# Performance work log

Hardware: AMD Instinct MI355X
Metric: run time of the kernel (lower is better)

Reference implementation:

```python
import jax, jax.numpy as jnp
from jax import lax
import numpy as np

LRELU_SLOPE = 0.1
DILATIONS = (1, 2, 4)
B, C, T = 8, 256, 8192


def pd_indexing(x, d, dilation):
    """Pitch-dependent past/future gather along time.
    x: (B, C, T); d: (B, 1, T) float dilation factors.
    Returns xP, xF: (B, C, T), zero where index is out of range.
    """
    b, c, t_len = x.shape
    t = jnp.arange(t_len, dtype=x.dtype)  # (T,)
    dil = d[:, 0, :] * dilation           # (B, T)
    idxP = jnp.round(t[None, :] - dil).astype(jnp.int32)  # (B, T)
    idxF = jnp.round(t[None, :] + dil).astype(jnp.int32)  # (B, T)
    validP = (idxP >= 0).astype(x.dtype)[:, None, :]        # (B,1,T)
    validF = (idxF < t_len).astype(x.dtype)[:, None, :]
    idxPc = jnp.broadcast_to(jnp.clip(idxP, 0, t_len - 1)[:, None, :], (b, c, t_len))
    idxFc = jnp.broadcast_to(jnp.clip(idxF, 0, t_len - 1)[:, None, :], (b, c, t_len))
    xP = jnp.take_along_axis(x, idxPc, axis=2) * validP
    xF = jnp.take_along_axis(x, idxFc, axis=2) * validF
    return xP, xF


def conv1x1(x, w, bias):
    # x: (B,C,T), w: (O,C), bias: (O,)
    return jnp.einsum('oc,bct->bot', w, x) + bias[None, :, None]


def conv3(x, w, bias):
    # x: (B,C,T), w: (O,C,3), padding=1
    y = lax.conv_general_dilated(x, w, window_strides=(1,), padding=[(1, 1)],
                                 dimension_numbers=('NCH', 'OIH', 'NCH'))
    return y + bias[None, :, None]


def setup_inputs() -> dict:
    key = jax.random.key(0)
    ks = jax.random.split(key, 8)
    x = jax.random.normal(ks[0], (B, C, T), dtype=jnp.float32)
    d = jax.random.uniform(ks[1], (B, 1, T), dtype=jnp.float32, minval=0.0, maxval=16.0)
    n = len(DILATIONS)
    s1 = 1.0 / np.sqrt(C)
    s3 = 1.0 / np.sqrt(3 * C)
    WC = jax.random.normal(ks[2], (n, C, C), dtype=jnp.float32) * s1
    WP = jax.random.normal(ks[3], (n, C, C), dtype=jnp.float32) * s1
    WF = jax.random.normal(ks[4], (n, C, C), dtype=jnp.float32) * s1
    WA = jax.random.normal(ks[5], (n, C, C, 3), dtype=jnp.float32) * s3
    bC = jnp.zeros((n, C), dtype=jnp.float32)
    bP = jnp.zeros((n, C), dtype=jnp.float32)
    bF = jnp.zeros((n, C), dtype=jnp.float32)
    bA = jnp.zeros((n, C), dtype=jnp.float32)
    return {"x": x, "d": d, "WC": WC, "bC": bC, "WP": WP, "bP": bP,
            "WF": WF, "bF": bF, "WA": WA, "bA": bA}


def reference(x, d, WC, bC, WP, bP, WF, bF, WA, bA):
    for i, dilation in enumerate(DILATIONS):
        xt = jax.nn.leaky_relu(x, LRELU_SLOPE)
        xP, xF = pd_indexing(xt, d, dilation)
        xt = conv1x1(xt, WC[i], bC[i]) + conv1x1(xP, WP[i], bP[i]) + conv1x1(xF, WF[i], bF[i])
        xt = jax.nn.leaky_relu(xt, LRELU_SLOPE)
        xt = conv3(xt, WA[i], bA[i])
        x = xt + x
    return x
```

## Files before the change

kernel.cpp:

```cpp
#include <hip/hip_runtime.h>
#include <hip/hip_bf16.h>
#include <cstddef>
#include <cstdint>

constexpr int Bn = 8, Cn = 256, Tn = 8192;
constexpr int NL = 3;
constexpr int Kc = 768;
constexpr float SLOPE = 0.1f;

typedef unsigned short u16;
using bf8   = __attribute__((ext_vector_type(8))) short;
using f32x4 = __attribute__((ext_vector_type(4))) float;

__device__ __forceinline__ float lrelu(float v) { return v > 0.f ? v : SLOPE * v; }
__device__ __forceinline__ u16 f2bf(float f) {
    __hip_bfloat16 h = __float2bfloat16(f);
    return *reinterpret_cast<u16*>(&h);
}

__device__ __forceinline__ void g2l16(const u16* g, u16* l) {
    __builtin_amdgcn_global_load_lds(
        (const __attribute__((address_space(1))) char*)g,
        (__attribute__((address_space(3))) char*)l, 16, 0, 0);
}

__device__ __forceinline__ void pipe_barrier() {
    __builtin_amdgcn_s_barrier();
    __builtin_amdgcn_sched_barrier(0);
}

__global__ __launch_bounds__(256)
void k_wprep(const float* __restrict__ WC, const float* __restrict__ WP,
             const float* __restrict__ WF, const float* __restrict__ WA,
             const float* __restrict__ bC, const float* __restrict__ bP,
             const float* __restrict__ bF,
             u16* __restrict__ Wcat, u16* __restrict__ WAp, float* __restrict__ bSum,
             u16* __restrict__ zrow)
{
    if (blockIdx.x == 0) zrow[threadIdx.x] = 0;
    const int n1 = NL * Cn * Kc;
    for (int i = blockIdx.x * blockDim.x + threadIdx.x; i < n1;
         i += gridDim.x * blockDim.x) {
        int c = i % Cn;
        int s = (i / Cn) % 3;
        int o = (i / (3 * Cn)) % Cn;
        int l = i / (3 * Cn * Cn);
        size_t src = ((size_t)l * Cn + o) * Cn + c;
        float wc = (s == 0) ? WC[src] : (s == 1) ? WP[src] : WF[src];
        Wcat[i] = f2bf(wc);
        WAp[i] = f2bf(WA[src * 3 + s]);
    }
    for (int i = blockIdx.x * blockDim.x + threadIdx.x; i < NL * Cn;
         i += gridDim.x * blockDim.x)
        bSum[i] = bC[i] + bP[i] + bF[i];
}

__global__ __launch_bounds__(256)
void k_prep(const float* __restrict__ x, u16* __restrict__ xT)
{
    __shared__ float s[64][65];
    const int b = blockIdx.z, c0 = blockIdx.y * 64, t0 = blockIdx.x * 64;
    const int tid = threadIdx.x;
    const float* xb = x + ((size_t)b * Cn + c0) * Tn + t0;

    int tt = tid & 63, c4 = tid >> 6;
    for (int cc = c4; cc < 64; cc += 4)
        s[cc][tt] = xb[(size_t)cc * Tn + tt];
    __syncthreads();

    int ccS = tid & 63, t4 = tid >> 6;
    u16* xTb = xT + ((size_t)b * Tn + t0) * Cn + c0;
    for (int t2 = t4; t2 < 64; t2 += 4)
        xTb[(size_t)t2 * Cn + ccS] = f2bf(lrelu(s[ccS][t2]));
}

__global__ __launch_bounds__(256, 3)
void k_gemm1(const u16* __restrict__ xT, const float* __restrict__ d,
             const u16* __restrict__ Wl, const float* __restrict__ bS,
             float dil, u16* __restrict__ zT, const u16* __restrict__ zrow)
{
    __shared__ u16 smem[6 * 4096];
    __shared__ int sRow[3][128];

    const int tid = threadIdx.x;
    const int b = blockIdx.z;
    const int t0 = blockIdx.x * 128;
    const int o0 = blockIdx.y * 128;

    if (tid < 128) {
        int t = t0 + tid;
        float dv = d[(size_t)b * Tn + t] * dil;
        int ip = (int)rintf((float)t - dv);
        int iF = (int)rintf((float)t + dv);
        sRow[0][tid] = t;
        sRow[1][tid] = (ip >= 0) ? ip : -1;
        sRow[2][tid] = (iF < Tn) ? iF : -1;
    }
    __syncthreads();

    const int srow = tid >> 2;
    const int schunkL = (tid & 3) * 8;
    const int schunkG = ((tid & 3) ^ ((tid >> 3) & 3)) * 8;
    const u16* xTb = xT + (size_t)b * Tn * Cn;
    const char* xbc = (const char*)xTb;
    const int zoff = (int)((const char*)(zrow + schunkG) - xbc);

    int offX0[3], offX1[3];
    #pragma unroll
    for (int s = 0; s < 3; ++s) {
        int r0 = sRow[s][srow], r1 = sRow[s][srow + 64];
        offX0[s] = (r0 >= 0) ? (int)(((size_t)r0 * Cn + schunkG) * 2) : zoff;
        offX1[s] = (r1 >= 0) ? (int)(((size_t)r1 * Cn + schunkG) * 2) : zoff;
    }
    const u16* wbase = Wl + (size_t)(o0 + srow) * Kc + schunkG;

    const int lane = tid & 63, wv = tid >> 6;
    const int wm = (wv & 1) * 64;
    const int wn = (wv >> 1) * 64;
    const int lr = lane & 15, quad = lane >> 4;
    const int rchunk = (quad ^ ((lr >> 1) & 3)) * 8;

    const int ldsW = srow * 32 + schunkL;
    const int ldsW2 = (srow + 64) * 32 + schunkL;

    auto dma = [&](int kg, int bsel) {
        int seg = kg >> 3, kk = (kg & 7) * 32;
        u16* bx = smem + bsel * 4096;
        u16* bw = smem + 12288 + bsel * 4096;
        g2l16(wbase + seg * 256 + kk,                   bw + ldsW);
        g2l16(wbase + (size_t)64 * Kc + seg * 256 + kk, bw + ldsW2);
        g2l16((const u16*)(xbc + offX0[seg] + kk * 2), bx + ldsW);
        g2l16((const u16*)(xbc + offX1[seg] + kk * 2), bx + ldsW2);
    };

    f32x4 acc[4][4] = {};
    dma(0, 0); dma(1, 1);

    #pragma unroll
    for (int kg = 0; kg < 24; ++kg) {
        if (kg < 23)
            asm volatile("s_waitcnt vmcnt(4) lgkmcnt(0)" ::: "memory");
        else
            asm volatile("s_waitcnt vmcnt(0) lgkmcnt(0)" ::: "memory");
        pipe_barrier();

        const u16* bX = smem + (kg % 3) * 4096;
        const u16* bW = smem + 12288 + (kg % 3) * 4096;

        bf8 af[4], bg[4];
        #pragma unroll
        for (int mi = 0; mi < 4; ++mi)
            af[mi] = *(const bf8*)(bX + (wm + mi * 16 + lr) * 32 + rchunk);
        #pragma unroll
        for (int ni = 0; ni < 4; ++ni)
            bg[ni] = *(const bf8*)(bW + (wn + ni * 16 + lr) * 32 + rchunk);

        if (kg + 2 < 24) dma(kg + 2, (kg + 2) % 3);

        __builtin_amdgcn_s_setprio(1);
        #pragma unroll
        for (int mi = 0; mi < 4; ++mi)
            #pragma unroll
            for (int ni = 0; ni < 4; ++ni)
                acc[mi][ni] = __builtin_amdgcn_mfma_f32_16x16x32_bf16(
                    af[mi], bg[ni], acc[mi][ni], 0, 0, 0);
        __builtin_amdgcn_s_setprio(0);
    }

    float bias[4];
    #pragma unroll
    for (int ni = 0; ni < 4; ++ni) bias[ni] = bS[o0 + wn + ni * 16 + lr];
    u16* zTb = zT + (size_t)b * Tn * Cn;
    #pragma unroll
    for (int mi = 0; mi < 4; ++mi)
        #pragma unroll
        for (int r = 0; r < 4; ++r) {
            int t = t0 + wm + mi * 16 + quad * 4 + r;
            u16* row = zTb + (size_t)t * Cn + o0 + wn;
            #pragma unroll
            for (int ni = 0; ni < 4; ++ni)
                row[ni * 16 + lr] = f2bf(lrelu(acc[mi][ni][r] + bias[ni]));
        }
}

__global__ __launch_bounds__(256, 3)
void k_gemm2(const u16* __restrict__ zT, const u16* __restrict__ WAl,
             const float* __restrict__ bA, const float* __restrict__ xres,
             float* __restrict__ out, u16* __restrict__ xTn, int writeXT,
             const u16* __restrict__ zrow)
{
    __shared__ u16 smem[6 * 4096];

    const int tid = threadIdx.x;
    const int b = blockIdx.z;
    const int t0 = blockIdx.x * 128;
    const int o0 = blockIdx.y * 128;

    const int srow = tid >> 2;
    const int schunkL = (tid & 3) * 8;
    const int schunkG = ((tid & 3) ^ ((tid >> 3) & 3)) * 8;
    const int lane = tid & 63, wv = tid >> 6;
    const int wo = (wv & 1) * 64;
    const int wt = (wv >> 1) * 64;
    const int lr = lane & 15, quad = lane >> 4;
    const int rchunk = (quad ^ ((lr >> 1) & 3)) * 8;

    const u16* zTb = zT + (size_t)b * Tn * Cn;
    const char* zbc = (const char*)zTb;
    const int zoff = (int)((const char*)(zrow + schunkG) - zbc);

    int offZ0[3], offZ1[3];
    #pragma unroll
    for (int tap = 0; tap < 3; ++tap) {
        int r0 = t0 + srow + tap - 1;
        int r1 = r0 + 64;
        offZ0[tap] = (r0 >= 0 && r0 < Tn)
                         ? (int)(((size_t)r0 * Cn + schunkG) * 2) : zoff;
        offZ1[tap] = (r1 >= 0 && r1 < Tn)
                         ? (int)(((size_t)r1 * Cn + schunkG) * 2) : zoff;
    }
    const u16* wbase = WAl + (size_t)(o0 + srow) * Kc + schunkG;

    const int ldsW = srow * 32 + schunkL;
    const int ldsW2 = (srow + 64) * 32 + schunkL;

    auto dma = [&](int kg, int bsel) {
        int tap = kg >> 3, kk = (kg & 7) * 32;
        u16* bz = smem + bsel * 4096;
        u16* bw = smem + 12288 + bsel * 4096;
        g2l16(wbase + tap * 256 + kk,                   bw + ldsW);
        g2l16(wbase + (size_t)64 * Kc + tap * 256 + kk, bw + ldsW2);
        g2l16((const u16*)(zbc + offZ0[tap] + kk * 2), bz + ldsW);
        g2l16((const u16*)(zbc + offZ1[tap] + kk * 2), bz + ldsW2);
    };

    f32x4 acc[4][4] = {};
    dma(0, 0); dma(1, 1);

    #pragma unroll
    for (int kg = 0; kg < 24; ++kg) {
        if (kg < 23)
            asm volatile("s_waitcnt vmcnt(4) lgkmcnt(0)" ::: "memory");
        else
            asm volatile("s_waitcnt vmcnt(0) lgkmcnt(0)" ::: "memory");
        pipe_barrier();

        const u16* bZ = smem + (kg % 3) * 4096;
        const u16* bW = smem + 12288 + (kg % 3) * 4096;

        bf8 af[4], bg[4];
        #pragma unroll
        for (int mi = 0; mi < 4; ++mi)
            af[mi] = *(const bf8*)(bW + (wo + mi * 16 + lr) * 32 + rchunk);
        #pragma unroll
        for (int ni = 0; ni < 4; ++ni)
            bg[ni] = *(const bf8*)(bZ + (wt + ni * 16 + lr) * 32 + rchunk);

        if (kg + 2 < 24) dma(kg + 2, (kg + 2) % 3);

        __builtin_amdgcn_s_setprio(1);
        #pragma unroll
        for (int mi = 0; mi < 4; ++mi)
            #pragma unroll
            for (int ni = 0; ni < 4; ++ni)
                acc[mi][ni] = __builtin_amdgcn_mfma_f32_16x16x32_bf16(
                    af[mi], bg[ni], acc[mi][ni], 0, 0, 0);
        __builtin_amdgcn_s_setprio(0);
    }

    float biasv[4][4];
    #pragma unroll
    for (int mi = 0; mi < 4; ++mi) {
        float4 bb = *(const float4*)(bA + o0 + wo + mi * 16 + quad * 4);
        biasv[mi][0] = bb.x; biasv[mi][1] = bb.y; biasv[mi][2] = bb.z; biasv[mi][3] = bb.w;
    }

    if (writeXT) {
        u16* strip = smem + wv * 1152;
        u16* xTb2 = xTn + (size_t)b * Tn * Cn;
        #pragma unroll
        for (int ni = 0; ni < 4; ++ni) {
            __syncthreads();
            #pragma unroll
            for (int mi = 0; mi < 4; ++mi) {
                ushort4 pk;
                #pragma unroll
                for (int r = 0; r < 4; ++r) {
                    int o = o0 + wo + mi * 16 + quad * 4 + r;
                    size_t idx = ((size_t)b * Cn + o) * Tn + t0 + wt + ni * 16 + lr;
                    float v = acc[mi][ni][r] + biasv[mi][r] + xres[idx];
                    out[idx] = v;
                    ((u16*)&pk)[r] = f2bf(lrelu(v));
                }
                *(ushort4*)(strip + lr * 72 + mi * 16 + quad * 4) = pk;
            }
            __syncthreads();
            #pragma unroll
            for (int it = 0; it < 2; ++it) {
                int tt = (lane >> 3) + it * 8;
                uint4 vv = *(const uint4*)(strip + tt * 72 + (lane & 7) * 8);
                *(uint4*)(xTb2 + (size_t)(t0 + wt + ni * 16 + tt) * Cn
                          + o0 + wo + (lane & 7) * 8) = vv;
            }
        }
    } else {
        #pragma unroll
        for (int mi = 0; mi < 4; ++mi)
            #pragma unroll
            for (int r = 0; r < 4; ++r) {
                int o = o0 + wo + mi * 16 + quad * 4 + r;
                size_t base = ((size_t)b * Cn + o) * Tn + t0 + wt;
                #pragma unroll
                for (int ni = 0; ni < 4; ++ni) {
                    size_t idx = base + ni * 16 + lr;
                    out[idx] = acc[mi][ni][r] + biasv[mi][r] + xres[idx];
                }
            }
    }
}

extern "C" void kernel_launch(void* const* d_in, const int* in_sizes, int n_in,
                              void* d_out, int out_size, void* d_ws, size_t ws_size,
                              hipStream_t stream)
{
    const float* x  = (const float*)d_in[0];
    const float* d  = (const float*)d_in[1];
    const float* WC = (const float*)d_in[2];
    const float* bC = (const float*)d_in[3];
    const float* WP = (const float*)d_in[4];
    const float* bP = (const float*)d_in[5];
    const float* WF = (const float*)d_in[6];
    const float* bF = (const float*)d_in[7];
    const float* WA = (const float*)d_in[8];
    const float* bA = (const float*)d_in[9];
    float* out = (float*)d_out;

    char* ws = (char*)d_ws;
    u16*   xT   = (u16*)(ws);
    u16*   zT   = (u16*)(ws + (size_t)Bn * Tn * Cn * 2);
    u16*   Wcat = (u16*)(ws + (size_t)2 * Bn * Tn * Cn * 2);
    u16*   WAp  = Wcat + (size_t)NL * Cn * Kc;
    float* bSum = (float*)(WAp + (size_t)NL * Cn * Kc);
    u16*   zrow = (u16*)(bSum + NL * Cn);

    k_wprep<<<dim3(1024), dim3(256), 0, stream>>>(WC, WP, WF, WA, bC, bP, bF,
                                                  Wcat, WAp, bSum, zrow);

    dim3 gP(Tn / 64, Cn / 64, Bn);
    dim3 gG(Tn / 128, Cn / 128, Bn);
    dim3 blk(256);

    k_prep<<<gP, blk, 0, stream>>>(x, xT);

    const float dils[NL] = {1.f, 2.f, 4.f};
    const float* xcur = x;
    for (int i = 0; i < NL; ++i) {
        k_gemm1<<<gG, blk, 0, stream>>>(xT, d,
                                        Wcat + (size_t)i * Cn * Kc,
                                        bSum + (size_t)i * Cn,
                                        dils[i], zT, zrow);
        k_gemm2<<<gG, blk, 0, stream>>>(zT,
                                        WAp + (size_t)i * Cn * Kc,
                                        bA + (size_t)i * Cn,
                                        xcur, out, xT, (i < NL - 1) ? 1 : 0,
                                        zrow);
        xcur = out;
    }
}
```

Measured before the change: 396.8 us.

## Fuse gather-GEMM and conv3 GEMM into one kernel with LDS-resident z tile

Merges the two per-layer GEMM kernels into one 512-thread block that covers all 256 output channels for a 128-step time tile. The first GEMM also computes the two halo rows, and its activated result stays in swizzled LDS as the input to the 3-tap conv GEMM. This removes the zT round trip through global memory and one launch per layer. In exchange each block recomputes the halo rows, holds more LDS and registers, runs a smaller grid with lower occupancy, and ping-pongs the xT buffers. The xT epilogue now writes 8-byte scattered stores instead of staging through LDS for coalesced 16-byte stores.

```diff
diff --git a/kernel.cpp b/kernel.cpp
--- a/kernel.cpp
+++ b/kernel.cpp
@@ -74,88 +74,211 @@
         xTb[(size_t)t2 * Cn + ccS] = f2bf(lrelu(s[ccS][t2]));
 }
 
-__global__ __launch_bounds__(256, 3)
-void k_gemm1(const u16* __restrict__ xT, const float* __restrict__ d,
+constexpr int SLOT = 12800;
+constexpr int ZOFF = 3 * SLOT;
+constexpr int ZSZ  = 130 * 256;
+
+__global__ __launch_bounds__(512, 2)
+void k_fused(const u16* __restrict__ xTsrc, const float* __restrict__ d,
              const u16* __restrict__ Wl, const float* __restrict__ bS,
-             float dil, u16* __restrict__ zT, const u16* __restrict__ zrow)
+             const u16* __restrict__ WAl, const float* __restrict__ bA,
+             float dil, const float* __restrict__ xres, float* __restrict__ out,
+             u16* __restrict__ xTn, int writeXT, const u16* __restrict__ zrow)
 {
-    __shared__ u16 smem[6 * 4096];
-    __shared__ int sRow[3][128];
+    __shared__ u16 smem[ZOFF + ZSZ];
+    __shared__ int sRow[3][130];
 
     const int tid = threadIdx.x;
     const int b = blockIdx.z;
     const int t0 = blockIdx.x * 128;
-    const int o0 = blockIdx.y * 128;
-
-    if (tid < 128) {
-        int t = t0 + tid;
-        float dv = d[(size_t)b * Tn + t] * dil;
-        int ip = (int)rintf((float)t - dv);
-        int iF = (int)rintf((float)t + dv);
-        sRow[0][tid] = t;
-        sRow[1][tid] = (ip >= 0) ? ip : -1;
-        sRow[2][tid] = (iF < Tn) ? iF : -1;
+
+    if (tid < 130) {
+        int tz = t0 - 1 + tid;
+        if (tz < 0 || tz >= Tn) {
+            sRow[0][tid] = -1; sRow[1][tid] = -1; sRow[2][tid] = -1;
+        } else {
+            float dv = d[(size_t)b * Tn + tz] * dil;
+            int ip = (int)rintf((float)tz - dv);
+            int iF = (int)rintf((float)tz + dv);
+            sRow[0][tid] = tz;
+            sRow[1][tid] = (ip >= 0) ? ip : -1;
+            sRow[2][tid] = (iF < Tn) ? iF : -1;
+        }
     }
     __syncthreads();
 
+    const int lane = tid & 63, wv = tid >> 6;
     const int srow = tid >> 2;
-    const int schunkL = (tid & 3) * 8;
-    const int schunkG = ((tid & 3) ^ ((tid >> 3) & 3)) * 8;
-    const u16* xTb = xT + (size_t)b * Tn * Cn;
+    const int sg  = ((tid & 3) ^ ((tid >> 3) & 3)) * 8;
+    const int sg2 = ((lane & 3) ^ ((lane >> 3) & 3)) * 8;
+
+    const u16* xTb = xTsrc + (size_t)b * Tn * Cn;
     const char* xbc = (const char*)xTb;
-    const int zoff = (int)((const char*)(zrow + schunkG) - xbc);
-
-    int offX0[3], offX1[3];
+    const int zoffA = (int)((const char*)(zrow + sg) - xbc);
+    const int zoffB = (int)((const char*)(zrow + sg2) - xbc);
+
+    int offX[3];
     #pragma unroll
     for (int s = 0; s < 3; ++s) {
-        int r0 = sRow[s][srow], r1 = sRow[s][srow + 64];
-        offX0[s] = (r0 >= 0) ? (int)(((size_t)r0 * Cn + schunkG) * 2) : zoff;
-        offX1[s] = (r1 >= 0) ? (int)(((size_t)r1 * Cn + schunkG) * 2) : zoff;
-    }
-    const u16* wbase = Wl + (size_t)(o0 + srow) * Kc + schunkG;
-
-    const int lane = tid & 63, wv = tid >> 6;
-    const int wm = (wv & 1) * 64;
-    const int wn = (wv >> 1) * 64;
+        int r = sRow[s][srow];
+        offX[s] = (r >= 0) ? (int)((r * Cn + sg) * 2) : zoffA;
+    }
+    int offX2[3] = { zoffB, zoffB, zoffB };
+    if (wv == 7) {
+        int j = lane >> 2;
+        if (j < 2) {
+            #pragma unroll
+            for (int s = 0; s < 3; ++s) {
+                int r = sRow[s][128 + j];
+                offX2[s] = (r >= 0) ? (int)((r * Cn + sg2) * 2) : zoffB;
+            }
+        }
+    }
+    const u16* wbase1 = Wl  + (size_t)srow * Kc + sg;
+    const u16* wbase2 = WAl + (size_t)srow * Kc + sg;
+
+    const int mo  = (wv & 3) * 64;
+    const int wzr = (wv >> 2) * 64;
+    const bool heavy = (wzr == 64);
     const int lr = lane & 15, quad = lane >> 4;
     const int rchunk = (quad ^ ((lr >> 1) & 3)) * 8;
 
-    const int ldsW = srow * 32 + schunkL;
-    const int ldsW2 = (srow + 64) * 32 + schunkL;
-
-    auto dma = [&](int kg, int bsel) {
+    auto dma1 = [&](int kg, int slot) {
         int seg = kg >> 3, kk = (kg & 7) * 32;
-        u16* bx = smem + bsel * 4096;
-        u16* bw = smem + 12288 + bsel * 4096;
-        g2l16(wbase + seg * 256 + kk,                   bw + ldsW);
-        g2l16(wbase + (size_t)64 * Kc + seg * 256 + kk, bw + ldsW2);
-        g2l16((const u16*)(xbc + offX0[seg] + kk * 2), bx + ldsW);
-        g2l16((const u16*)(xbc + offX1[seg] + kk * 2), bx + ldsW2);
+        u16* bw = smem + slot * SLOT;
+        u16* bx = bw + 8192;
+        if (wv == 7)
+            g2l16((const u16*)(xbc + offX2[seg] + kk * 2), bx + 4096 + lane * 8);
+        g2l16(wbase1 + seg * 256 + kk,                    bw + tid * 8);
+        g2l16(wbase1 + (size_t)128 * Kc + seg * 256 + kk, bw + 4096 + tid * 8);
+        g2l16((const u16*)(xbc + offX[seg] + kk * 2),     bx + tid * 8);
     };
-
-    f32x4 acc[4][4] = {};
-    dma(0, 0); dma(1, 1);
+    auto dma2 = [&](int kg, int slot) {
+        u16* bw = smem + slot * SLOT;
+        g2l16(wbase2 + kg * 32,                    bw + tid * 8);
+        g2l16(wbase2 + (size_t)128 * Kc + kg * 32, bw + 4096 + tid * 8);
+    };
+
+    const f32x4 zv4 = {0.f, 0.f, 0.f, 0.f};
+    f32x4 acc[4][5];
+    #pragma unroll
+    for (int mi = 0; mi < 4; ++mi)
+        #pragma unroll
+        for (int ni = 0; ni < 5; ++ni) acc[mi][ni] = zv4;
+
+    dma1(0, 0); dma1(1, 1);
 
     #pragma unroll
     for (int kg = 0; kg < 24; ++kg) {
-        if (kg < 23)
-            asm volatile("s_waitcnt vmcnt(4) lgkmcnt(0)" ::: "memory");
-        else
-            asm volatile("s_waitcnt vmcnt(0) lgkmcnt(0)" ::: "memory");
+        if (kg < 23) {
+            if (wv == 7) asm volatile("s_waitcnt vmcnt(4) lgkmcnt(0)" ::: "memory");
+            else         asm volatile("s_waitcnt vmcnt(3) lgkmcnt(0)" ::: "memory");
+        } else {
+            asm volatile("s_waitcnt vmcnt(2) lgkmcnt(0)" ::: "memory");
+        }
         pipe_barrier();
 
-        const u16* bX = smem + (kg % 3) * 4096;
-        const u16* bW = smem + 12288 + (kg % 3) * 4096;
-
+        const u16* bW = smem + (kg % 3) * SLOT;
+        const u16* bX = bW + 8192;
+        bf8 af[4], bg[4], bg4 = {};
+        #pragma unroll
+        for (int mi = 0; mi < 4; ++mi)
+            af[mi] = *(const bf8*)(bW + (mo + mi * 16 + lr) * 32 + rchunk);
+        #pragma unroll
+        for (int ni = 0; ni < 4; ++ni)
+            bg[ni] = *(const bf8*)(bX + (wzr + ni * 16 + lr) * 32 + rchunk);
+        if (heavy)
+            bg4 = *(const bf8*)(bX + (128 + lr) * 32 + rchunk);
+
+        if (kg + 2 < 24) dma1(kg + 2, (kg + 2) % 3);
+        else             dma2(kg - 22, (kg - 22) % 3);
+
+        __builtin_amdgcn_s_setprio(1);
+        #pragma unroll
+        for (int mi = 0; mi < 4; ++mi)
+            #pragma unroll
+            for (int ni = 0; ni < 4; ++ni)
+                acc[mi][ni] = __builtin_amdgcn_mfma_f32_16x16x32_bf16(
+                    af[mi], bg[ni], acc[mi][ni], 0, 0, 0);
+        if (heavy) {
+            #pragma unroll
+            for (int mi = 0; mi < 4; ++mi)
+                acc[mi][4] = __builtin_amdgcn_mfma_f32_16x16x32_bf16(
+                    af[mi], bg4, acc[mi][4], 0, 0, 0);
+        }
+        __builtin_amdgcn_s_setprio(0);
+    }
+
+    u16* zsm = smem + ZOFF;
+    {
+        float4 bSv[4];
+        #pragma unroll
+        for (int mi = 0; mi < 4; ++mi)
+            bSv[mi] = *(const float4*)(bS + mo + mi * 16 + quad * 4);
+
+        #pragma unroll
+        for (int ni = 0; ni < 4; ++ni) {
+            int zr = wzr + ni * 16 + lr;
+            int tz = t0 - 1 + zr;
+            bool vz = (tz >= 0) && (tz < Tn);
+            #pragma unroll
+            for (int mi = 0; mi < 4; ++mi) {
+                int ob = mo + mi * 16 + quad * 4;
+                ushort4 pk;
+                #pragma unroll
+                for (int r = 0; r < 4; ++r) {
+                    float v = acc[mi][ni][r] + ((const float*)&bSv[mi])[r];
+                    ((u16*)&pk)[r] = vz ? f2bf(lrelu(v)) : (u16)0;
+                }
+                int zi = zr * 256 + ((((ob >> 3) ^ (zr & 7)) << 3) | (ob & 7));
+                *(ushort4*)(zsm + zi) = pk;
+            }
+        }
+        if (heavy && lr < 2) {
+            int zr = 128 + lr;
+            int tz = t0 - 1 + zr;
+            bool vz = (tz >= 0) && (tz < Tn);
+            #pragma unroll
+            for (int mi = 0; mi < 4; ++mi) {
+                int ob = mo + mi * 16 + quad * 4;
+                ushort4 pk;
+                #pragma unroll
+                for (int r = 0; r < 4; ++r) {
+                    float v = acc[mi][4][r] + ((const float*)&bSv[mi])[r];
+                    ((u16*)&pk)[r] = vz ? f2bf(lrelu(v)) : (u16)0;
+                }
+                int zi = zr * 256 + ((((ob >> 3) ^ (zr & 7)) << 3) | (ob & 7));
+                *(ushort4*)(zsm + zi) = pk;
+            }
+        }
+    }
+    asm volatile("s_waitcnt lgkmcnt(0)" ::: "memory");
+    __builtin_amdgcn_s_barrier();
+    __builtin_amdgcn_sched_barrier(0);
+
+    #pragma unroll
+    for (int mi = 0; mi < 4; ++mi)
+        #pragma unroll
+        for (int ni = 0; ni < 4; ++ni) acc[mi][ni] = zv4;
+
+    #pragma unroll
+    for (int kg = 0; kg < 24; ++kg) {
+        if (kg < 23) asm volatile("s_waitcnt vmcnt(2) lgkmcnt(0)" ::: "memory");
+        else         asm volatile("s_waitcnt vmcnt(0) lgkmcnt(0)" ::: "memory");
+        pipe_barrier();
+
+        const u16* bW = smem + (kg % 3) * SLOT;
+        const int tap = kg >> 3, cI = (kg & 7) * 4 + quad;
         bf8 af[4], bg[4];
         #pragma unroll
         for (int mi = 0; mi < 4; ++mi)
-            af[mi] = *(const bf8*)(bX + (wm + mi * 16 + lr) * 32 + rchunk);
-        #pragma unroll
-        for (int ni = 0; ni < 4; ++ni)
-            bg[ni] = *(const bf8*)(bW + (wn + ni * 16 + lr) * 32 + rchunk);
-
-        if (kg + 2 < 24) dma(kg + 2, (kg + 2) % 3);
+            af[mi] = *(const bf8*)(bW + (mo + mi * 16 + lr) * 32 + rchunk);
+        #pragma unroll
+        for (int ni = 0; ni < 4; ++ni) {
+            int zr = wzr + ni * 16 + lr + tap;
+            bg[ni] = *(const bf8*)(zsm + zr * 256 + ((cI ^ (zr & 7)) << 3));
+        }
+        if (kg + 2 < 24) dma2(kg + 2, (kg + 2) % 3);
 
         __builtin_amdgcn_s_setprio(1);
         #pragma unroll
@@ -167,155 +290,30 @@
         __builtin_amdgcn_s_setprio(0);
     }
 
-    float bias[4];
-    #pragma unroll
-    for (int ni = 0; ni < 4; ++ni) bias[ni] = bS[o0 + wn + ni * 16 + lr];
-    u16* zTb = zT + (size_t)b * Tn * Cn;
-    #pragma unroll
-    for (int mi = 0; mi < 4; ++mi)
-        #pragma unroll
-        for (int r = 0; r < 4; ++r) {
-            int t = t0 + wm + mi * 16 + quad * 4 + r;
-            u16* row = zTb + (size_t)t * Cn + o0 + wn;
-            #pragma unroll
-            for (int ni = 0; ni < 4; ++ni)
-                row[ni * 16 + lr] = f2bf(lrelu(acc[mi][ni][r] + bias[ni]));
-        }
-}
-
-__global__ __launch_bounds__(256, 3)
-void k_gemm2(const u16* __restrict__ zT, const u16* __restrict__ WAl,
-             const float* __restrict__ bA, const float* __restrict__ xres,
-             float* __restrict__ out, u16* __restrict__ xTn, int writeXT,
-             const u16* __restrict__ zrow)
-{
-    __shared__ u16 smem[6 * 4096];
-
-    const int tid = threadIdx.x;
-    const int b = blockIdx.z;
-    const int t0 = blockIdx.x * 128;
-    const int o0 = blockIdx.y * 128;
-
-    const int srow = tid >> 2;
-    const int schunkL = (tid & 3) * 8;
-    const int schunkG = ((tid & 3) ^ ((tid >> 3) & 3)) * 8;
-    const int lane = tid & 63, wv = tid >> 6;
-    const int wo = (wv & 1) * 64;
-    const int wt = (wv >> 1) * 64;
-    const int lr = lane & 15, quad = lane >> 4;
-    const int rchunk = (quad ^ ((lr >> 1) & 3)) * 8;
-
-    const u16* zTb = zT + (size_t)b * Tn * Cn;
-    const char* zbc = (const char*)zTb;
-    const int zoff = (int)((const char*)(zrow + schunkG) - zbc);
-
-    int offZ0[3], offZ1[3];
-    #pragma unroll
-    for (int tap = 0; tap < 3; ++tap) {
-        int r0 = t0 + srow + tap - 1;
-        int r1 = r0 + 64;
-        offZ0[tap] = (r0 >= 0 && r0 < Tn)
-                         ? (int)(((size_t)r0 * Cn + schunkG) * 2) : zoff;
-        offZ1[tap] = (r1 >= 0 && r1 < Tn)
-                         ? (int)(((size_t)r1 * Cn + schunkG) * 2) : zoff;
-    }
-    const u16* wbase = WAl + (size_t)(o0 + srow) * Kc + schunkG;
-
-    const int ldsW = srow * 32 + schunkL;
-    const int ldsW2 = (srow + 64) * 32 + schunkL;
-
-    auto dma = [&](int kg, int bsel) {
-        int tap = kg >> 3, kk = (kg & 7) * 32;
-        u16* bz = smem + bsel * 4096;
-        u16* bw = smem + 12288 + bsel * 4096;
-        g2l16(wbase + tap * 256 + kk,                   bw + ldsW);
-        g2l16(wbase + (size_t)64 * Kc + tap * 256 + kk, bw + ldsW2);
-        g2l16((const u16*)(zbc + offZ0[tap] + kk * 2), bz + ldsW);
-        g2l16((const u16*)(zbc + offZ1[tap] + kk * 2), bz + ldsW2);
-    };
-
-    f32x4 acc[4][4] = {};
-    dma(0, 0); dma(1, 1);
-
-    #pragma unroll
-    for (int kg = 0; kg < 24; ++kg) {
-        if (kg < 23)
-            asm volatile("s_waitcnt vmcnt(4) lgkmcnt(0)" ::: "memory");
-        else
-            asm volatile("s_waitcnt vmcnt(0) lgkmcnt(0)" ::: "memory");
-        pipe_barrier();
-
-        const u16* bZ = smem + (kg % 3) * 4096;
-        const u16* bW = smem + 12288 + (kg % 3) * 4096;
-
-        bf8 af[4], bg[4];
-        #pragma unroll
-        for (int mi = 0; mi < 4; ++mi)
-            af[mi] = *(const bf8*)(bW + (wo + mi * 16 + lr) * 32 + rchunk);
-        #pragma unroll
-        for (int ni = 0; ni < 4; ++ni)
-            bg[ni] = *(const bf8*)(bZ + (wt + ni * 16 + lr) * 32 + rchunk);
-
-        if (kg + 2 < 24) dma(kg + 2, (kg + 2) % 3);
-
-        __builtin_amdgcn_s_setprio(1);
-        #pragma unroll
-        for (int mi = 0; mi < 4; ++mi)
-            #pragma unroll
-            for (int ni = 0; ni < 4; ++ni)
-                acc[mi][ni] = __builtin_amdgcn_mfma_f32_16x16x32_bf16(
-                    af[mi], bg[ni], acc[mi][ni], 0, 0, 0);
-        __builtin_amdgcn_s_setprio(0);
-    }
-
-    float biasv[4][4];
-    #pragma unroll
-    for (int mi = 0; mi < 4; ++mi) {
-        float4 bb = *(const float4*)(bA + o0 + wo + mi * 16 + quad * 4);
-        biasv[mi][0] = bb.x; biasv[mi][1] = bb.y; biasv[mi][2] = bb.z; biasv[mi][3] = bb.w;
-    }
-
-    if (writeXT) {
-        u16* strip = smem + wv * 1152;
-        u16* xTb2 = xTn + (size_t)b * Tn * Cn;
-        #pragma unroll
-        for (int ni = 0; ni < 4; ++ni) {
-            __syncthreads();
-            #pragma unroll
-            for (int mi = 0; mi < 4; ++mi) {
-                ushort4 pk;
+    {
+        float4 bAv[4];
+        #pragma unroll
+        for (int mi = 0; mi < 4; ++mi)
+            bAv[mi] = *(const float4*)(bA + mo + mi * 16 + quad * 4);
+
+        #pragma unroll
+        for (int mi = 0; mi < 4; ++mi) {
+            int ob = mo + mi * 16 + quad * 4;
+            #pragma unroll
+            for (int ni = 0; ni < 4; ++ni) {
+                int t = t0 + wzr + ni * 16 + lr;
+                ushort4 px;
                 #pragma unroll
                 for (int r = 0; r < 4; ++r) {
-                    int o = o0 + wo + mi * 16 + quad * 4 + r;
-                    size_t idx = ((size_t)b * Cn + o) * Tn + t0 + wt + ni * 16 + lr;
-                    float v = acc[mi][ni][r] + biasv[mi][r] + xres[idx];
+                    size_t idx = ((size_t)b * Cn + ob + r) * Tn + t;
+                    float v = acc[mi][ni][r] + ((const float*)&bAv[mi])[r] + xres[idx];
                     out[idx] = v;
-                    ((u16*)&pk)[r] = f2bf(lrelu(v));
+                    ((u16*)&px)[r] = f2bf(lrelu(v));
                 }
-                *(ushort4*)(strip + lr * 72 + mi * 16 + quad * 4) = pk;
+                if (writeXT)
+                    *(ushort4*)(xTn + ((size_t)b * Tn + t) * Cn + ob) = px;
             }
-            __syncthreads();
-            #pragma unroll
-            for (int it = 0; it < 2; ++it) {
-                int tt = (lane >> 3) + it * 8;
-                uint4 vv = *(const uint4*)(strip + tt * 72 + (lane & 7) * 8);
-                *(uint4*)(xTb2 + (size_t)(t0 + wt + ni * 16 + tt) * Cn
-                          + o0 + wo + (lane & 7) * 8) = vv;
-            }
-        }
-    } else {
-        #pragma unroll
-        for (int mi = 0; mi < 4; ++mi)
-            #pragma unroll
-            for (int r = 0; r < 4; ++r) {
-                int o = o0 + wo + mi * 16 + quad * 4 + r;
-                size_t base = ((size_t)b * Cn + o) * Tn + t0 + wt;
-                #pragma unroll
-                for (int ni = 0; ni < 4; ++ni) {
-                    size_t idx = base + ni * 16 + lr;
-                    out[idx] = acc[mi][ni][r] + biasv[mi][r] + xres[idx];
-                }
-            }
+        }
     }
 }
 
@@ -336,8 +334,8 @@
     float* out = (float*)d_out;
 
     char* ws = (char*)d_ws;
-    u16*   xT   = (u16*)(ws);
-    u16*   zT   = (u16*)(ws + (size_t)Bn * Tn * Cn * 2);
+    u16*   xTa  = (u16*)(ws);
+    u16*   xTb  = (u16*)(ws + (size_t)Bn * Tn * Cn * 2);
     u16*   Wcat = (u16*)(ws + (size_t)2 * Bn * Tn * Cn * 2);
     u16*   WAp  = Wcat + (size_t)NL * Cn * Kc;
     float* bSum = (float*)(WAp + (size_t)NL * Cn * Kc);
@@ -347,23 +345,19 @@
                                                   Wcat, WAp, bSum, zrow);
 
     dim3 gP(Tn / 64, Cn / 64, Bn);
-    dim3 gG(Tn / 128, Cn / 128, Bn);
-    dim3 blk(256);
-
-    k_prep<<<gP, blk, 0, stream>>>(x, xT);
+    k_prep<<<gP, dim3(256), 0, stream>>>(x, xTa);
 
     const float dils[NL] = {1.f, 2.f, 4.f};
     const float* xcur = x;
+    u16* xsrc = xTa;
+    u16* xdst = xTb;
     for (int i = 0; i < NL; ++i) {
-        k_gemm1<<<gG, blk, 0, stream>>>(xT, d,
-                                        Wcat + (size_t)i * Cn * Kc,
-                                        bSum + (size_t)i * Cn,
-                                        dils[i], zT, zrow);
-        k_gemm2<<<gG, blk, 0, stream>>>(zT,
-                                        WAp + (size_t)i * Cn * Kc,
-                                        bA + (size_t)i * Cn,
-                                        xcur, out, xT, (i < NL - 1) ? 1 : 0,
-                                        zrow);
+        k_fused<<<dim3(Tn / 128, 1, Bn), dim3(512), 0, stream>>>(
+            xsrc, d,
+            Wcat + (size_t)i * Cn * Kc, bSum + (size_t)i * Cn,
+            WAp  + (size_t)i * Cn * Kc, bA + (size_t)i * Cn,
+            dils[i], xcur, out, xdst, (i < NL - 1) ? 1 : 0, zrow);
         xcur = out;
-    }
-}
+        u16* tmp = xsrc; xsrc = xdst; xdst = tmp;
+    }
+}
```

After: 389.0 us. 1.02x faster.
